# Kernel optimization log

Measured on AMD Instinct MI355X. Metric: run time of the kernel, lower is better.

## Reference

```python
import jax, jax.numpy as jnp
import numpy as np

B, N, E = 8, 5000, 100000
IN_DIM, OUT_DIM = 128, 128
EPS = 1e-5


def setup_inputs() -> dict:
    key = jax.random.key(0)
    ks = jax.random.split(key, 8)
    node_features = jax.random.normal(ks[0], (B, N, IN_DIM), dtype=jnp.float32)
    edge_index = jax.random.randint(ks[1], (B, 2, E), 0, N, dtype=jnp.int32)
    node_mask = jnp.ones((B, N), dtype=jnp.float32)
    edge_mask = jnp.ones((B, E), dtype=jnp.float32)
    s = 1.0 / np.sqrt(IN_DIM)
    W_self = jax.random.uniform(ks[2], (IN_DIM, OUT_DIM), minval=-s, maxval=s, dtype=jnp.float32)
    b_self = jax.random.uniform(ks[3], (OUT_DIM,), minval=-s, maxval=s, dtype=jnp.float32)
    W_nb = jax.random.uniform(ks[4], (IN_DIM, OUT_DIM), minval=-s, maxval=s, dtype=jnp.float32)
    b_nb = jax.random.uniform(ks[5], (OUT_DIM,), minval=-s, maxval=s, dtype=jnp.float32)
    gamma = jnp.ones((OUT_DIM,), dtype=jnp.float32)
    beta = jnp.zeros((OUT_DIM,), dtype=jnp.float32)
    return {"node_features": node_features, "edge_index": edge_index,
            "node_mask": node_mask, "edge_mask": edge_mask,
            "W_self": W_self, "b_self": b_self, "W_nb": W_nb, "b_nb": b_nb,
            "gamma": gamma, "beta": beta}


def _aggregate_mean(x, ei, em):
    # x: [N, D], ei: [2, E], em: [E]. Masked segment-mean over incoming edges.
    src, tgt = ei[0], ei[1]
    sf = x[src] * em[:, None]                                   # [E, D]
    sums = jax.ops.segment_sum(sf, tgt, num_segments=N)         # [N, D]
    cnt = jax.ops.segment_sum(em, tgt, num_segments=N)          # [N]
    return sums / jnp.maximum(cnt, 1.0)[:, None]


def reference(node_features, edge_index, node_mask, edge_mask,
              W_self, b_self, W_nb, b_nb, gamma, beta):
    self_feat = jnp.einsum('bnd,do->bno', node_features, W_self) + b_self
    agg = jax.vmap(_aggregate_mean)(node_features, edge_index, edge_mask)  # [B,N,D]
    nb_feat = jnp.einsum('bnd,do->bno', agg, W_nb) + b_nb
    out = jax.nn.relu(self_feat + nb_feat)
    # dropout in eval mode -> identity
    mu = jnp.mean(out, axis=-1, keepdims=True)
    var = jnp.var(out, axis=-1, keepdims=True)
    out = (out - mu) * jax.lax.rsqrt(var + EPS) * gamma + beta
    return out * node_mask[..., None]
```

## Files before the change

### kernel.cpp

```cpp
#include <hip/hip_runtime.h>


#define B_ 8
#define N_ 5000
#define E_ 100000
#define D_ 128
#define EPS_ 1e-5f
#define NNODES (B_ * N_)
#define NEDGES (B_ * E_)
#define JB 313
#define PPB ((E_ / 2 + 255) / 256)
#define FILL_BLOCKS (8 * PPB)
#define CONV_BLOCKS 2500
#define CAP 64
#define LDSP 136
#define GATHER_BLOCKS (NNODES / 4)

typedef __bf16 bf16x8 __attribute__((ext_vector_type(8)));
typedef float  f32x4  __attribute__((ext_vector_type(4)));

static __device__ __forceinline__ unsigned short f2bf(float f) {
    union { float f; unsigned int i; } c; c.f = f;
    unsigned int i = c.i;
    i += 0x7fffu + ((i >> 16) & 1u);
    return (unsigned short)(i >> 16);
}
static __device__ __forceinline__ float bflo(unsigned int u) {
    return __uint_as_float(u << 16);
}
static __device__ __forceinline__ float bfhi(unsigned int u) {
    return __uint_as_float(u & 0xffff0000u);
}

__global__ __launch_bounds__(256) void fill_k(
    const int* __restrict__ ei, const float* __restrict__ em,
    int* __restrict__ cnt, unsigned int* __restrict__ entries,
    const float* __restrict__ x, unsigned short* __restrict__ xbf,
    const float* __restrict__ Wself, const float* __restrict__ Wnb,
    unsigned short* __restrict__ Bt)
{
    int blk = blockIdx.x;
    if (blk < FILL_BLOCKS) {
        int b = blk & 7;
        int p = (blk >> 3) * 256 + threadIdx.x;
        if (p >= E_ / 2) return;
        int e = 2 * p;
        const int* eib = ei + (size_t)b * 2 * E_;
        int2   sv = *(const int2*)(eib + e);
        int2   tv = *(const int2*)(eib + E_ + e);
        float2 mv = *(const float2*)(em + (size_t)b * E_ + e);
        int gb = b * N_;
        int g0 = gb + tv.x, g1 = gb + tv.y;
        int e0 = (mv.x != 0.0f), e1 = (mv.y != 0.0f);
        int s0 = atomicAdd(&cnt[g0], e0);
        int s1 = atomicAdd(&cnt[g1], e1);
        if (e0 && s0 < CAP)
            entries[((size_t)g0 << 6) + s0] =
                (unsigned int)(gb + sv.x) | ((unsigned int)f2bf(mv.x) << 16);
        if (e1 && s1 < CAP)
            entries[((size_t)g1 << 6) + s1] =
                (unsigned int)(gb + sv.y) | ((unsigned int)f2bf(mv.y) << 16);
    } else if (blk < FILL_BLOCKS + CONV_BLOCKS) {
        size_t base = (size_t)(blk - FILL_BLOCKS) * 2048 + threadIdx.x * 8;
        float4 va = *(const float4*)(x + base);
        float4 vb = *(const float4*)(x + base + 4);
        uint4 o;
        o.x = (unsigned int)f2bf(va.x) | ((unsigned int)f2bf(va.y) << 16);
        o.y = (unsigned int)f2bf(va.z) | ((unsigned int)f2bf(va.w) << 16);
        o.z = (unsigned int)f2bf(vb.x) | ((unsigned int)f2bf(vb.y) << 16);
        o.w = (unsigned int)f2bf(vb.z) | ((unsigned int)f2bf(vb.w) << 16);
        *(uint4*)(xbf + base) = o;
    } else {
        int n = blk - FILL_BLOCKS - CONV_BLOCKS;
        int k = threadIdx.x;
        float v = (k < 128) ? Wself[(size_t)k * D_ + n]
                            : Wnb[(size_t)(k - 128) * D_ + n];
        Bt[(size_t)n * 256 + k] = f2bf(v);
    }
}

__global__ __launch_bounds__(256) void gather_k(
    const unsigned short* __restrict__ xbf, const int* __restrict__ cnt,
    const unsigned int* __restrict__ entries, unsigned short* __restrict__ aggbf)
{
    int t = threadIdx.x;
    int lane = t & 63, wv = t >> 6;
    int g = (blockIdx.x & 7) * N_ + (blockIdx.x >> 3) * 4 + wv;

    int sq = lane >> 4;
    int c8 = lane & 15;

    int dg = cnt[g]; if (dg > CAP) dg = CAP;
    unsigned int ee = entries[((size_t)g << 6) + lane];

    float a[8];
    #pragma unroll
    for (int i = 0; i < 8; ++i) a[i] = 0.f;
    float cs = 0.f;

    uint4 v[8]; float mj[8];
    #pragma unroll
    for (int q = 0; q < 8; ++q) {
        unsigned int ej = (unsigned int)__shfl((int)ee, 4 * q + sq, 64);
        int ok = 4 * q + sq < dg;
        int sj = ok ? (int)(ej & 0xffffu) : 0;
        mj[q] = ok ? __uint_as_float(ej & 0xffff0000u) : 0.0f;
        v[q] = *(const uint4*)(xbf + ((size_t)sj << 7) + (c8 << 3));
    }
    #pragma unroll
    for (int q = 0; q < 8; ++q) {
        if (4 * q < dg) {
            float m = mj[q];
            a[0] += bflo(v[q].x) * m; a[1] += bfhi(v[q].x) * m;
            a[2] += bflo(v[q].y) * m; a[3] += bfhi(v[q].y) * m;
            a[4] += bflo(v[q].z) * m; a[5] += bfhi(v[q].z) * m;
            a[6] += bflo(v[q].w) * m; a[7] += bfhi(v[q].w) * m;
            cs += m;
        }
    }
    if (dg > 32) {
        #pragma unroll 1
        for (int q = 8; q < 16; ++q) {
            if (4 * q >= dg) break;
            unsigned int ej = (unsigned int)__shfl((int)ee, 4 * q + sq, 64);
            int ok = 4 * q + sq < dg;
            int sj = ok ? (int)(ej & 0xffffu) : 0;
            float m = ok ? __uint_as_float(ej & 0xffff0000u) : 0.0f;
            uint4 w = *(const uint4*)(xbf + ((size_t)sj << 7) + (c8 << 3));
            a[0] += bflo(w.x) * m; a[1] += bfhi(w.x) * m;
            a[2] += bflo(w.y) * m; a[3] += bfhi(w.y) * m;
            a[4] += bflo(w.z) * m; a[5] += bfhi(w.z) * m;
            a[6] += bflo(w.w) * m; a[7] += bfhi(w.w) * m;
            cs += m;
        }
    }

    #pragma unroll
    for (int i = 0; i < 8; ++i) {
        a[i] += __shfl_xor(a[i], 16, 64);
        a[i] += __shfl_xor(a[i], 32, 64);
    }
    cs += __shfl_xor(cs, 16, 64);
    cs += __shfl_xor(cs, 32, 64);

    if (lane < 16) {
        float inv = 1.0f / fmaxf(cs, 1.0f);
        uint4 o;
        o.x = (unsigned int)f2bf(a[0] * inv) | ((unsigned int)f2bf(a[1] * inv) << 16);
        o.y = (unsigned int)f2bf(a[2] * inv) | ((unsigned int)f2bf(a[3] * inv) << 16);
        o.z = (unsigned int)f2bf(a[4] * inv) | ((unsigned int)f2bf(a[5] * inv) << 16);
        o.w = (unsigned int)f2bf(a[6] * inv) | ((unsigned int)f2bf(a[7] * inv) << 16);
        *(uint4*)(aggbf + ((size_t)g << 7) + (c8 << 3)) = o;
    }
}

__global__ __launch_bounds__(256) void gemm_k(
    const unsigned short* __restrict__ xbf, const unsigned short* __restrict__ aggbf,
    const unsigned short* __restrict__ Bt,
    const float* __restrict__ bself, const float* __restrict__ bnb,
    const float* __restrict__ gamma, const float* __restrict__ beta,
    const float* __restrict__ nmask, float* __restrict__ out)
{
    __shared__ unsigned short xs[16][LDSP];
    __shared__ unsigned short as[16][LDSP];
    __shared__ float red[4][2][16];

    int t = threadIdx.x;
    int lane = t & 63, wv = t >> 6;
    int b = blockIdx.x & 7;
    int j = blockIdx.x >> 3;
    int i0 = j * 16;
    int g0 = b * N_ + i0;
    int limit = N_ - i0; if (limit > 16) limit = 16;

    #pragma unroll
    for (int lr = wv * 4; lr < wv * 4 + 4; ++lr) {
        unsigned int vx = 0, va = 0;
        if (lr < limit) {
            vx = ((const unsigned int*)(xbf + (size_t)(g0 + lr) * D_))[lane];
            va = ((const unsigned int*)(aggbf + (size_t)(g0 + lr) * D_))[lane];
        }
        ((unsigned int*)&xs[lr][0])[lane] = vx;
        ((unsigned int*)&as[lr][0])[lane] = va;
    }
    __syncthreads();

    int quad = lane >> 4;
    int lcol = lane & 15;

    f32x4 acc[2];
    acc[0] = (f32x4)0.0f;
    acc[1] = (f32x4)0.0f;

    #pragma unroll
    for (int kk = 0; kk < 4; ++kk) {
        int kof = kk * 32 + quad * 8;
        bf16x8 av = *(const bf16x8*)&xs[lcol][kof];
        #pragma unroll
        for (int p = 0; p < 2; ++p) {
            int tt = wv * 2 + p;
            bf16x8 bf = *(const bf16x8*)(Bt + (size_t)(tt * 16 + lcol) * 256 + kof);
            acc[p] = __builtin_amdgcn_mfma_f32_16x16x32_bf16(av, bf, acc[p], 0, 0, 0);
        }
    }
    #pragma unroll
    for (int kk = 0; kk < 4; ++kk) {
        int kof = kk * 32 + quad * 8;
        bf16x8 av = *(const bf16x8*)&as[lcol][kof];
        #pragma unroll
        for (int p = 0; p < 2; ++p) {
            int tt = wv * 2 + p;
            bf16x8 bf = *(const bf16x8*)(Bt + (size_t)(tt * 16 + lcol) * 256 + 128 + kof);
            acc[p] = __builtin_amdgcn_mfma_f32_16x16x32_bf16(av, bf, acc[p], 0, 0, 0);
        }
    }

    float h[2][4];
    float s[4] = {0, 0, 0, 0}, q[4] = {0, 0, 0, 0};
    float gam[2], bet[2];
    #pragma unroll
    for (int p = 0; p < 2; ++p) {
        int col = (wv * 2 + p) * 16 + lcol;
        float bs = bself[col] + bnb[col];
        gam[p] = gamma[col];
        bet[p] = beta[col];
        #pragma unroll
        for (int r = 0; r < 4; ++r) {
            float v = fmaxf(acc[p][r] + bs, 0.0f);
            h[p][r] = v;
            s[r] += v;
            q[r] += v * v;
        }
    }
    #pragma unroll
    for (int r = 0; r < 4; ++r) {
        #pragma unroll
        for (int off = 1; off <= 8; off <<= 1) {
            s[r] += __shfl_xor(s[r], off, 64);
            q[r] += __shfl_xor(q[r], off, 64);
        }
    }
    if (lcol == 0) {
        #pragma unroll
        for (int r = 0; r < 4; ++r) {
            red[wv][0][quad * 4 + r] = s[r];
            red[wv][1][quad * 4 + r] = q[r];
        }
    }
    __syncthreads();

    #pragma unroll
    for (int r = 0; r < 4; ++r) {
        int row = quad * 4 + r;
        int irow = i0 + row;
        if (irow >= N_) continue;
        float S = red[0][0][row] + red[1][0][row] + red[2][0][row] + red[3][0][row];
        float Q = red[0][1][row] + red[1][1][row] + red[2][1][row] + red[3][1][row];
        float mu = S * (1.0f / D_);
        float var = Q * (1.0f / D_) - mu * mu;
        float rin = rsqrtf(fmaxf(var, 0.0f) + EPS_);
        int g = b * N_ + irow;
        float mk = nmask[g];
        float* op = out + (size_t)g * D_;
        #pragma unroll
        for (int p = 0; p < 2; ++p) {
            int col = (wv * 2 + p) * 16 + lcol;
            op[col] = ((h[p][r] - mu) * rin * gam[p] + bet[p]) * mk;
        }
    }
}

extern "C" void kernel_launch(void* const* d_in, const int* in_sizes, int n_in,
                              void* d_out, int out_size, void* d_ws, size_t ws_size,
                              hipStream_t stream)
{
    const float* x     = (const float*)d_in[0];
    const int*   ei    = (const int*)d_in[1];
    const float* nmask = (const float*)d_in[2];
    const float* em    = (const float*)d_in[3];
    const float* Wself = (const float*)d_in[4];
    const float* bself = (const float*)d_in[5];
    const float* Wnb   = (const float*)d_in[6];
    const float* bnb   = (const float*)d_in[7];
    const float* gamma = (const float*)d_in[8];
    const float* beta  = (const float*)d_in[9];
    float* out = (float*)d_out;

    int* cnt = (int*)d_ws;
    unsigned int* entries = (unsigned int*)(cnt + NNODES);
    unsigned short* Bt = (unsigned short*)(entries + (size_t)NNODES * CAP);
    unsigned short* xbf = Bt + (size_t)128 * 256;
    unsigned short* aggbf = xbf + (size_t)NNODES * D_;

    hipMemsetAsync(cnt, 0, NNODES * sizeof(int), stream);
    fill_k<<<FILL_BLOCKS + CONV_BLOCKS + 128, 256, 0, stream>>>(
        ei, em, cnt, entries, x, xbf, Wself, Wnb, Bt);
    gather_k<<<GATHER_BLOCKS, 256, 0, stream>>>(xbf, cnt, entries, aggbf);
    gemm_k<<<8 * JB, 256, 0, stream>>>(xbf, aggbf, Bt,
                                       bself, bnb, gamma, beta, nmask, out);
}
```

Measured before the change: 171.9 us.

## Fuse neighbor gather into GEMM kernel with double-buffered LDS DMA staging

Merges the gather/mean-aggregation kernel into the GEMM+layernorm kernel, so aggregated features go straight into LDS instead of making a bf16 round trip through global memory. The neighbor rows are fetched with global_load_lds DMA into a double-buffered per-wave stage buffer, and explicit vmcnt waits overlap the next row's loads with the current row's accumulation. This saves one kernel launch and the aggbf write and read. In exchange it adds 32KB of LDS per block, which lowers occupancy, and the gather now runs at the GEMM grid's coarser granularity.

```diff
diff --git a/kernel.cpp b/kernel.cpp
--- a/kernel.cpp
+++ b/kernel.cpp
@@ -7,14 +7,12 @@
 #define D_ 128
 #define EPS_ 1e-5f
 #define NNODES (B_ * N_)
-#define NEDGES (B_ * E_)
 #define JB 313
 #define PPB ((E_ / 2 + 255) / 256)
 #define FILL_BLOCKS (8 * PPB)
 #define CONV_BLOCKS 2500
 #define CAP 64
 #define LDSP 136
-#define GATHER_BLOCKS (NNODES / 4)
 
 typedef __bf16 bf16x8 __attribute__((ext_vector_type(8)));
 typedef float  f32x4  __attribute__((ext_vector_type(4)));
@@ -31,6 +29,18 @@
 static __device__ __forceinline__ float bfhi(unsigned int u) {
     return __uint_as_float(u & 0xffff0000u);
 }
+
+static __device__ __forceinline__ void dma16(const unsigned short* g,
+                                             unsigned short* l) {
+    __builtin_amdgcn_global_load_lds(
+        (const __attribute__((address_space(1))) unsigned int*)g,
+        (__attribute__((address_space(3))) unsigned int*)l,
+        16, 0, 0);
+}
+#define WAITVM8() do { asm volatile("s_waitcnt vmcnt(8)" ::: "memory"); \
+                       __builtin_amdgcn_sched_barrier(0); } while (0)
+#define WAITVM0() do { asm volatile("s_waitcnt vmcnt(0)" ::: "memory"); \
+                       __builtin_amdgcn_sched_barrier(0); } while (0)
 
 __global__ __launch_bounds__(256) void fill_k(
     const int* __restrict__ ei, const float* __restrict__ em,
@@ -79,83 +89,9 @@
     }
 }
 
-__global__ __launch_bounds__(256) void gather_k(
+__global__ __launch_bounds__(256) void fused_k(
     const unsigned short* __restrict__ xbf, const int* __restrict__ cnt,
-    const unsigned int* __restrict__ entries, unsigned short* __restrict__ aggbf)
-{
-    int t = threadIdx.x;
-    int lane = t & 63, wv = t >> 6;
-    int g = (blockIdx.x & 7) * N_ + (blockIdx.x >> 3) * 4 + wv;
-
-    int sq = lane >> 4;
-    int c8 = lane & 15;
-
-    int dg = cnt[g]; if (dg > CAP) dg = CAP;
-    unsigned int ee = entries[((size_t)g << 6) + lane];
-
-    float a[8];
-    #pragma unroll
-    for (int i = 0; i < 8; ++i) a[i] = 0.f;
-    float cs = 0.f;
-
-    uint4 v[8]; float mj[8];
-    #pragma unroll
-    for (int q = 0; q < 8; ++q) {
-        unsigned int ej = (unsigned int)__shfl((int)ee, 4 * q + sq, 64);
-        int ok = 4 * q + sq < dg;
-        int sj = ok ? (int)(ej & 0xffffu) : 0;
-        mj[q] = ok ? __uint_as_float(ej & 0xffff0000u) : 0.0f;
-        v[q] = *(const uint4*)(xbf + ((size_t)sj << 7) + (c8 << 3));
-    }
-    #pragma unroll
-    for (int q = 0; q < 8; ++q) {
-        if (4 * q < dg) {
-            float m = mj[q];
-            a[0] += bflo(v[q].x) * m; a[1] += bfhi(v[q].x) * m;
-            a[2] += bflo(v[q].y) * m; a[3] += bfhi(v[q].y) * m;
-            a[4] += bflo(v[q].z) * m; a[5] += bfhi(v[q].z) * m;
-            a[6] += bflo(v[q].w) * m; a[7] += bfhi(v[q].w) * m;
-            cs += m;
-        }
-    }
-    if (dg > 32) {
-        #pragma unroll 1
-        for (int q = 8; q < 16; ++q) {
-            if (4 * q >= dg) break;
-            unsigned int ej = (unsigned int)__shfl((int)ee, 4 * q + sq, 64);
-            int ok = 4 * q + sq < dg;
-            int sj = ok ? (int)(ej & 0xffffu) : 0;
-            float m = ok ? __uint_as_float(ej & 0xffff0000u) : 0.0f;
-            uint4 w = *(const uint4*)(xbf + ((size_t)sj << 7) + (c8 << 3));
-            a[0] += bflo(w.x) * m; a[1] += bfhi(w.x) * m;
-            a[2] += bflo(w.y) * m; a[3] += bfhi(w.y) * m;
-            a[4] += bflo(w.z) * m; a[5] += bfhi(w.z) * m;
-            a[6] += bflo(w.w) * m; a[7] += bfhi(w.w) * m;
-            cs += m;
-        }
-    }
-
-    #pragma unroll
-    for (int i = 0; i < 8; ++i) {
-        a[i] += __shfl_xor(a[i], 16, 64);
-        a[i] += __shfl_xor(a[i], 32, 64);
-    }
-    cs += __shfl_xor(cs, 16, 64);
-    cs += __shfl_xor(cs, 32, 64);
-
-    if (lane < 16) {
-        float inv = 1.0f / fmaxf(cs, 1.0f);
-        uint4 o;
-        o.x = (unsigned int)f2bf(a[0] * inv) | ((unsigned int)f2bf(a[1] * inv) << 16);
-        o.y = (unsigned int)f2bf(a[2] * inv) | ((unsigned int)f2bf(a[3] * inv) << 16);
-        o.z = (unsigned int)f2bf(a[4] * inv) | ((unsigned int)f2bf(a[5] * inv) << 16);
-        o.w = (unsigned int)f2bf(a[6] * inv) | ((unsigned int)f2bf(a[7] * inv) << 16);
-        *(uint4*)(aggbf + ((size_t)g << 7) + (c8 << 3)) = o;
-    }
-}
-
-__global__ __launch_bounds__(256) void gemm_k(
-    const unsigned short* __restrict__ xbf, const unsigned short* __restrict__ aggbf,
+    const unsigned int* __restrict__ entries,
     const unsigned short* __restrict__ Bt,
     const float* __restrict__ bself, const float* __restrict__ bnb,
     const float* __restrict__ gamma, const float* __restrict__ beta,
@@ -164,6 +100,7 @@
     __shared__ unsigned short xs[16][LDSP];
     __shared__ unsigned short as[16][LDSP];
     __shared__ float red[4][2][16];
+    __shared__ unsigned short stage[4][2][32][128];
 
     int t = threadIdx.x;
     int lane = t & 63, wv = t >> 6;
@@ -173,16 +110,100 @@
     int g0 = b * N_ + i0;
     int limit = N_ - i0; if (limit > 16) limit = 16;
 
+    int sq = lane >> 4;
+    int c8 = lane & 15;
+
+    int dg4[4]; unsigned int ee4[4];
+    #pragma unroll
+    for (int i = 0; i < 4; ++i) {
+        int row = wv * 4 + i;
+        int gi = g0 + ((row < limit) ? row : 0);
+        int d = cnt[gi]; if (d > CAP) d = CAP;
+        dg4[i] = (row < limit) ? d : 0;
+        ee4[i] = entries[((size_t)gi << 6) + lane];
+    }
+
     #pragma unroll
     for (int lr = wv * 4; lr < wv * 4 + 4; ++lr) {
-        unsigned int vx = 0, va = 0;
-        if (lr < limit) {
-            vx = ((const unsigned int*)(xbf + (size_t)(g0 + lr) * D_))[lane];
-            va = ((const unsigned int*)(aggbf + (size_t)(g0 + lr) * D_))[lane];
-        }
-        ((unsigned int*)&xs[lr][0])[lane] = vx;
-        ((unsigned int*)&as[lr][0])[lane] = va;
-    }
+        unsigned int v = 0;
+        if (lr < limit)
+            v = ((const unsigned int*)(xbf + (size_t)(g0 + lr) * D_))[lane];
+        ((unsigned int*)&xs[lr][0])[lane] = v;
+    }
+
+#define STAGE(I, BB) do {                                                     \
+        _Pragma("unroll")                                                     \
+        for (int q = 0; q < 8; ++q) {                                         \
+            unsigned int ej = (unsigned int)__shfl((int)ee4[I], 4 * q + sq, 64); \
+            int okq = (4 * q + sq) < dg4[I];                                  \
+            int srow = okq ? (int)(ej & 0xffffu) : 0;                         \
+            dma16(xbf + ((size_t)srow << 7) + (c8 << 3),                      \
+                  &stage[wv][BB][4 * q][0]);                                  \
+        }                                                                     \
+    } while (0)
+
+    STAGE(0, 0);
+
+    #pragma unroll
+    for (int i = 0; i < 4; ++i) {
+        if (i == 0) STAGE(1, 1);
+        else if (i == 1) STAGE(2, 0);
+        else if (i == 2) STAGE(3, 1);
+
+        if (i < 3) { WAITVM8(); } else { WAITVM0(); }
+
+        float a[8];
+        #pragma unroll
+        for (int z = 0; z < 8; ++z) a[z] = 0.f;
+        float cs = 0.f;
+        #pragma unroll
+        for (int q = 0; q < 8; ++q) {
+            unsigned int ej = (unsigned int)__shfl((int)ee4[i], 4 * q + sq, 64);
+            int okq = (4 * q + sq) < dg4[i];
+            float m = okq ? __uint_as_float(ej & 0xffff0000u) : 0.0f;
+            uint4 v = *(const uint4*)&stage[wv][i & 1][4 * q + sq][c8 << 3];
+            a[0] += bflo(v.x) * m; a[1] += bfhi(v.x) * m;
+            a[2] += bflo(v.y) * m; a[3] += bfhi(v.y) * m;
+            a[4] += bflo(v.z) * m; a[5] += bfhi(v.z) * m;
+            a[6] += bflo(v.w) * m; a[7] += bfhi(v.w) * m;
+            cs += m;
+        }
+        if (__builtin_expect(dg4[i] > 32, 0)) {
+            #pragma unroll 1
+            for (int q = 8; q < 16; ++q) {
+                if (4 * q >= dg4[i]) break;
+                unsigned int ej = (unsigned int)__shfl((int)ee4[i], 4 * q + sq, 64);
+                int okq = (4 * q + sq) < dg4[i];
+                int sj = okq ? (int)(ej & 0xffffu) : 0;
+                float m = okq ? __uint_as_float(ej & 0xffff0000u) : 0.0f;
+                uint4 w = *(const uint4*)(xbf + ((size_t)sj << 7) + (c8 << 3));
+                a[0] += bflo(w.x) * m; a[1] += bfhi(w.x) * m;
+                a[2] += bflo(w.y) * m; a[3] += bfhi(w.y) * m;
+                a[4] += bflo(w.z) * m; a[5] += bfhi(w.z) * m;
+                a[6] += bflo(w.w) * m; a[7] += bfhi(w.w) * m;
+                cs += m;
+            }
+        }
+
+        #pragma unroll
+        for (int z = 0; z < 8; ++z) {
+            a[z] += __shfl_xor(a[z], 16, 64);
+            a[z] += __shfl_xor(a[z], 32, 64);
+        }
+        cs += __shfl_xor(cs, 16, 64);
+        cs += __shfl_xor(cs, 32, 64);
+
+        if (lane < 16) {
+            float inv = 1.0f / fmaxf(cs, 1.0f);
+            uint4 o;
+            o.x = (unsigned int)f2bf(a[0] * inv) | ((unsigned int)f2bf(a[1] * inv) << 16);
+            o.y = (unsigned int)f2bf(a[2] * inv) | ((unsigned int)f2bf(a[3] * inv) << 16);
+            o.z = (unsigned int)f2bf(a[4] * inv) | ((unsigned int)f2bf(a[5] * inv) << 16);
+            o.w = (unsigned int)f2bf(a[6] * inv) | ((unsigned int)f2bf(a[7] * inv) << 16);
+            *(uint4*)&as[wv * 4 + i][c8 << 3] = o;
+        }
+    }
+#undef STAGE
     __syncthreads();
 
     int quad = lane >> 4;
@@ -290,12 +311,10 @@
     unsigned int* entries = (unsigned int*)(cnt + NNODES);
     unsigned short* Bt = (unsigned short*)(entries + (size_t)NNODES * CAP);
     unsigned short* xbf = Bt + (size_t)128 * 256;
-    unsigned short* aggbf = xbf + (size_t)NNODES * D_;
 
     hipMemsetAsync(cnt, 0, NNODES * sizeof(int), stream);
     fill_k<<<FILL_BLOCKS + CONV_BLOCKS + 128, 256, 0, stream>>>(
         ei, em, cnt, entries, x, xbf, Wself, Wnb, Bt);
-    gather_k<<<GATHER_BLOCKS, 256, 0, stream>>>(xbf, cnt, entries, aggbf);
-    gemm_k<<<8 * JB, 256, 0, stream>>>(xbf, aggbf, Bt,
-                                       bself, bnb, gamma, beta, nmask, out);
-}
+    fused_k<<<8 * JB, 256, 0, stream>>>(xbf, cnt, entries, Bt,
+                                        bself, bnb, gamma, beta, nmask, out);
+}
```

Result: slower. 185.6 us (+8.0%).
